# Performance work log

Measured on AMD Instinct MI355X. Metric: run time of the kernel, lower is better.

The kernel has to match this reference:

```python
import jax, jax.numpy as jnp
import numpy as np

HEADS = 8
BN_EPS = 1e-5

def _bn(x2d, g, b):
    # torch BatchNorm1d in training mode: biased batch stats
    mu = x2d.mean(0)
    var = x2d.var(0)
    return (x2d - mu) * jax.lax.rsqrt(var + BN_EPS) * g + b

def _window_indices(H):
    # exclusive-end box coordinates, in the exact order of the torch loop
    m = H // 2
    r0, r1, c0, c1 = [], [], [], []
    for i in range(1, m + 1):
        wins = [(m - i, m + i + 1, m - i, m + i + 1),  # full square
                (m - i, m + 1,     m - i, m + i + 1),  # top half
                (m,     m + i + 1, m - i, m + i + 1),  # bottom half
                (m - i, m + i + 1, m - i, m + 1),      # left half
                (m - i, m + i + 1, m,     m + i + 1)]  # right half
        for a, b, c, d in wins:
            r0.append(a); r1.append(b); c0.append(c); c1.append(d)
    r0 = np.array(r0); r1 = np.array(r1); c0 = np.array(c0); c1 = np.array(c1)
    counts = ((r1 - r0) * (c1 - c0)).astype(np.float32)
    return r0, r1, c0, c1, counts

def _box_sums(P, r0, r1, c0, c1):
    # P: padded 2D prefix sum [B, C, H+1, H+1]; returns [B, C, K]
    return P[:, :, r1, c1] - P[:, :, r0, c1] - P[:, :, r1, c0] + P[:, :, r0, c0]

def _integral(img):
    return jnp.pad(jnp.cumsum(jnp.cumsum(img, axis=2), axis=3), ((0, 0), (0, 0), (1, 0), (1, 0)))

def setup_inputs() -> dict:
    key = jax.random.key(0)
    ks = jax.random.split(key, 8)
    B, Cin, H = 64, 512, 31
    C = 512  # heads * base_dim
    x = jax.random.normal(ks[0], (B, Cin, H, H), dtype=jnp.float32)
    w_v = jax.random.normal(ks[1], (Cin, C), dtype=jnp.float32) * 0.02
    w_k = jax.random.normal(ks[2], (Cin, C), dtype=jnp.float32) * 0.02
    w_fc = jax.random.normal(ks[3], (Cin + C, 512), dtype=jnp.float32) * 0.02
    z = lambda n: jnp.zeros((n,), jnp.float32)
    o = lambda n: jnp.ones((n,), jnp.float32)
    return {"x": x,
            "w_v": w_v, "b_v": z(C), "g_vn": o(C), "b_vn": z(C),
            "w_k": w_k, "b_k": z(C), "g_kn": o(C), "b_kn": z(C),
            "w_fc": w_fc, "b_fc": z(512), "g_fcn": o(512), "b_fcn": z(512)}

def reference(x, w_v, b_v, g_vn, b_vn, w_k, b_k, g_kn, b_kn, w_fc, b_fc, g_fcn, b_fcn):
    B, Cin, H, W = x.shape
    N = H * W
    C = w_v.shape[1]
    d = C // HEADS
    m = H // 2
    xt = x.reshape(B, Cin, N).transpose(0, 2, 1)       # [B, N, Cin]
    x0 = xt[:, N // 2, :]                              # [B, Cin] center pixel feature
    flat = xt.reshape(B * N, Cin)
    v = jax.nn.relu(_bn(flat @ w_v + b_v, g_vn, b_vn))
    v = v.reshape(B, N, C).transpose(0, 2, 1).reshape(B, C, H, H)
    k = _bn(flat @ w_k + b_k, g_kn, b_kn).reshape(B, N, HEADS, d).transpose(0, 2, 1, 3)  # [B,h,N,d]
    q = k[:, :, N // 2, :]                             # [B, h, d]
    attn = jax.nn.softmax(jnp.einsum('bhd,bhnd->bhn', q, k) * (d ** -0.5), axis=-1)      # [B,h,N]
    attn_full = jnp.broadcast_to(attn[:, :, None, :], (B, HEADS, d, N)).reshape(B, C, H, H)
    xw = attn_full * v                                 # attn-weighted values [B,C,H,H]
    eps = 1e-16
    r0, r1, c0, c1, counts = _window_indices(H)
    Px = _integral(xw)
    Pa = _integral(attn_full)
    mx = _box_sums(Px, r0, r1, c0, c1) / counts        # window means of xw   [B,C,K]
    ma = _box_sums(Pa, r0, r1, c0, c1) / counts        # window means of attn [B,C,K]
    y_win = (mx / (ma + eps)).transpose(0, 2, 1)       # [B, K, C]
    y = jnp.concatenate([xw[:, :, m, m][:, None, :], y_win], axis=1)  # [B, n, C]
    # F.normalize(p=2, dim=2)
    y = y / jnp.maximum(jnp.linalg.norm(y, axis=2, keepdims=True), 1e-12)
    n = y.shape[1]
    yy = jnp.concatenate([jnp.broadcast_to(x0[:, None, :], (B, n, Cin)), y], axis=-1)
    out = jax.nn.relu(_bn(yy.reshape(B * n, Cin + C) @ w_fc + b_fc, g_fcn, b_fcn))
    return out.reshape(B, n, -1)
```

## Files before the change

kernel.cpp:

```cpp
#include <hip/hip_runtime.h>
#include <stdint.h>

#define DEV __device__ __forceinline__

typedef __bf16 bf16x8 __attribute__((ext_vector_type(8)));
typedef unsigned short u16x8 __attribute__((ext_vector_type(8)));
typedef float f32x4 __attribute__((ext_vector_type(4)));

DEV uint16_t f2bf(float f) {
    union { float f; uint32_t u; } v; v.f = f;
    uint32_t r = v.u + 0x7fffu + ((v.u >> 16) & 1u);
    return (uint16_t)(r >> 16);
}
DEV float bf2f(uint16_t h) {
    union { uint32_t u; float f; } v; v.u = ((uint32_t)h) << 16;
    return v.f;
}

#if __has_builtin(__builtin_amdgcn_global_load_lds)
DEV void async16(const uint16_t* g, uint16_t* l) {
    __builtin_amdgcn_global_load_lds(
        (const __attribute__((address_space(1))) uint32_t*)g,
        (__attribute__((address_space(3))) uint32_t*)l, 16, 0, 0);
}
#else
DEV void async16(const uint16_t* g, uint16_t* l) {
    *(u16x8*)l = *(const u16x8*)g;
}
#endif

__global__ void k_convert_x(const float* __restrict__ x, uint16_t* __restrict__ xbt) {
    __shared__ float tile[32][33];
    int b = blockIdx.z;
    int n0 = blockIdx.x * 32;
    int c0 = blockIdx.y * 32;
    int tx = threadIdx.x, ty = threadIdx.y;
    #pragma unroll
    for (int i = 0; i < 4; ++i) {
        int c = c0 + ty + 8 * i;
        int n = n0 + tx;
        float v = 0.f;
        if (n < 961) v = x[((size_t)b * 512 + c) * 961 + n];
        tile[ty + 8 * i][tx] = v;
    }
    __syncthreads();
    #pragma unroll
    for (int i = 0; i < 4; ++i) {
        int n = n0 + ty + 8 * i;
        if (n < 961)
            xbt[((size_t)b * 961 + n) * 512 + c0 + tx] = f2bf(tile[tx][ty + 8 * i]);
    }
}

__global__ void k_convert_wvk(const float* __restrict__ wv, const float* __restrict__ wk,
                              uint16_t* __restrict__ wvkt) {
    int idx = blockIdx.x * 256 + threadIdx.x;
    int j = idx >> 9, k = idx & 511;
    float v = (j < 512) ? wv[(size_t)k * 512 + j] : wk[(size_t)k * 512 + (j - 512)];
    wvkt[idx] = f2bf(v);
}
__global__ void k_convert_wfc(const float* __restrict__ wfc, uint16_t* __restrict__ wfct) {
    int idx = blockIdx.x * 256 + threadIdx.x;
    int j = idx >> 10, k = idx & 1023;
    wfct[idx] = f2bf(wfc[(size_t)k * 512 + j]);
}

template<int K, int EPI>
__global__ __launch_bounds__(256, 2)
void k_gemm(const uint16_t* __restrict__ A, const uint16_t* __restrict__ Bt,
            int M_real,
            uint16_t* __restrict__ out_v, uint16_t* __restrict__ out_k,
            float* __restrict__ out_f,
            float* __restrict__ colsum, float* __restrict__ colsq)
{
    __shared__ __align__(16) uint16_t sA[128 * 32];
    __shared__ __align__(16) uint16_t sB[128 * 32];
    __shared__ float sStat[256];

    const int tid = threadIdx.x;
    const int wave = tid >> 6, lane = tid & 63;
    const int quad = lane >> 4, l16 = lane & 15;
    const int m0 = blockIdx.y * 128;
    const int j0 = blockIdx.x * 128;
    const int wm = wave >> 1, wj = wave & 1;

    const f32x4 fzero = {0.f, 0.f, 0.f, 0.f};
    f32x4 acc[4][4];
    #pragma unroll
    for (int i = 0; i < 4; ++i)
        #pragma unroll
        for (int j = 0; j < 4; ++j) acc[i][j] = fzero;

    const int c0 = tid;
    const int mA0 = c0 >> 2, kq0 = c0 & 3;
    const int c1 = tid + 256;
    const int mA1 = c1 >> 2, kq1 = c1 & 3;

    const int KT = K / 32;
    for (int kt = 0; kt < KT; ++kt) {
        const uint16_t* Ak = A + (size_t)m0 * K + kt * 32;
        const uint16_t* Bk = Bt + (size_t)j0 * K + kt * 32;
        async16(Ak + (size_t)mA0 * K + kq0 * 8, &sA[c0 * 8]);
        async16(Bk + (size_t)mA0 * K + kq0 * 8, &sB[c0 * 8]);
        async16(Ak + (size_t)mA1 * K + kq1 * 8, &sA[c1 * 8]);
        async16(Bk + (size_t)mA1 * K + kq1 * 8, &sB[c1 * 8]);
        __syncthreads();
        bf16x8 af[4], bfr[4];
        #pragma unroll
        for (int i = 0; i < 4; ++i) {
            int m = wm * 64 + i * 16 + l16;
            u16x8 r = *(const u16x8*)&sA[m * 32 + quad * 8];
            af[i] = __builtin_bit_cast(bf16x8, r);
        }
        #pragma unroll
        for (int j = 0; j < 4; ++j) {
            int jj = wj * 64 + j * 16 + l16;
            u16x8 r = *(const u16x8*)&sB[jj * 32 + quad * 8];
            bfr[j] = __builtin_bit_cast(bf16x8, r);
        }
        #pragma unroll
        for (int i = 0; i < 4; ++i)
            #pragma unroll
            for (int j = 0; j < 4; ++j)
                acc[i][j] = __builtin_amdgcn_mfma_f32_16x16x32_bf16(af[i], bfr[j], acc[i][j], 0, 0, 0);
        __syncthreads();
    }

    sStat[tid] = 0.f;
    __syncthreads();

    #pragma unroll
    for (int j = 0; j < 4; ++j) {
        const int col_local = wj * 64 + j * 16 + l16;
        const int jg = j0 + col_local;
        float ls = 0.f, lq = 0.f;
        #pragma unroll
        for (int i = 0; i < 4; ++i) {
            const int rbase = m0 + wm * 64 + i * 16 + quad * 4;
            #pragma unroll
            for (int reg = 0; reg < 4; ++reg) {
                const int r = rbase + reg;
                const float val = acc[i][j][reg];
                if (r < M_real) {
                    ls += val; lq += val * val;
                    if constexpr (EPI == 0) {
                        unsigned b = (unsigned)r / 961u;
                        unsigned n = (unsigned)r - b * 961u;
                        uint16_t hv = f2bf(val);
                        if (jg < 512) out_v[((size_t)b * 512 + jg) * 961 + n] = hv;
                        else          out_k[((size_t)b * 512 + (jg - 512)) * 961 + n] = hv;
                    } else {
                        out_f[(size_t)r * 512 + jg] = val;
                    }
                }
            }
        }
        ls += __shfl_xor(ls, 16); lq += __shfl_xor(lq, 16);
        ls += __shfl_xor(ls, 32); lq += __shfl_xor(lq, 32);
        if (quad == 0) {
            atomicAdd(&sStat[col_local], ls);
            atomicAdd(&sStat[128 + col_local], lq);
        }
    }
    __syncthreads();
    if (tid < 128) atomicAdd(&colsum[j0 + tid], sStat[tid]);
    else           atomicAdd(&colsq[j0 + (tid & 127)], sStat[tid]);
}

__global__ void k_bnfin(const float* __restrict__ s, const float* __restrict__ q,
                        const float* __restrict__ g, const float* __restrict__ be,
                        float* __restrict__ a, float* __restrict__ b2, float invM) {
    int j = blockIdx.x * 256 + threadIdx.x;
    float mean = s[j] * invM;
    float var = q[j] * invM - mean * mean;
    float aa = g[j] * rsqrtf(var + 1e-5f);
    a[j] = aa;
    b2[j] = be[j] - mean * aa;
}

__global__ void k_attn(const uint16_t* __restrict__ kraw,
                       const float* __restrict__ avec, const float* __restrict__ bvec,
                       float* __restrict__ attn, float* __restrict__ maw)
{
    __shared__ float qa[64];
    __shared__ float s_qb;
    __shared__ float att[961];
    __shared__ float red[8];

    int bh = blockIdx.x;
    int b = bh >> 3, h = bh & 7;
    int tid = threadIdx.x;

    if (tid < 64) {
        int c = h * 64 + tid;
        float kr = bf2f(kraw[((size_t)b * 512 + c) * 961 + 480]);
        float a = avec[512 + c], bb = bvec[512 + c];
        float qv = kr * a + bb;
        qa[tid] = qv * a;
        float qb = qv * bb;
        for (int off = 32; off; off >>= 1) qb += __shfl_down(qb, off);
        if (tid == 0) s_qb = qb;
    }
    __syncthreads();

    float lg[4];
    float lmax = -1e30f;
    #pragma unroll
    for (int it = 0; it < 4; ++it) {
        int n = tid + it * 256;
        float dot = -1e30f;
        if (n < 961) {
            const uint16_t* kp = kraw + ((size_t)b * 512 + h * 64) * 961 + n;
            float acc = 0.f;
            #pragma unroll 16
            for (int dd = 0; dd < 64; ++dd)
                acc += qa[dd] * bf2f(kp[(size_t)dd * 961]);
            dot = (acc + s_qb) * 0.125f;
        }
        lg[it] = dot;
        lmax = fmaxf(lmax, dot);
    }
    for (int off = 32; off; off >>= 1) lmax = fmaxf(lmax, __shfl_xor(lmax, off));
    if ((tid & 63) == 0) red[tid >> 6] = lmax;
    __syncthreads();
    float bmax = fmaxf(fmaxf(red[0], red[1]), fmaxf(red[2], red[3]));

    float lsum = 0.f;
    #pragma unroll
    for (int it = 0; it < 4; ++it) {
        int n = tid + it * 256;
        if (n < 961) {
            float e = __expf(lg[it] - bmax);
            lg[it] = e;
            lsum += e;
        }
    }
    for (int off = 32; off; off >>= 1) lsum += __shfl_xor(lsum, off);
    if ((tid & 63) == 0) red[4 + (tid >> 6)] = lsum;
    __syncthreads();
    float inv = 1.f / (red[4] + red[5] + red[6] + red[7]);
    #pragma unroll
    for (int it = 0; it < 4; ++it) {
        int n = tid + it * 256;
        if (n < 961) {
            float v = lg[it] * inv;
            att[n] = v;
            attn[(size_t)bh * 961 + n] = v;
        }
    }
    __syncthreads();

    if (tid < 31) { float s = 0.f; for (int cc = 0; cc < 31; ++cc) { s += att[tid * 31 + cc]; att[tid * 31 + cc] = s; } }
    __syncthreads();
    if (tid < 31) { float s = 0.f; for (int rr = 0; rr < 31; ++rr) { s += att[rr * 31 + tid]; att[rr * 31 + tid] = s; } }
    __syncthreads();

    if (tid < 75) {
        int i = tid / 5 + 1, t = tid % 5;
        const int m = 15;
        int r0, r1, cc0, cc1;
        switch (t) {
            case 0: r0 = m - i; r1 = m + i + 1; cc0 = m - i; cc1 = m + i + 1; break;
            case 1: r0 = m - i; r1 = m + 1;     cc0 = m - i; cc1 = m + i + 1; break;
            case 2: r0 = m;     r1 = m + i + 1; cc0 = m - i; cc1 = m + i + 1; break;
            case 3: r0 = m - i; r1 = m + i + 1; cc0 = m - i; cc1 = m + 1;     break;
            default:r0 = m - i; r1 = m + i + 1; cc0 = m;     cc1 = m + i + 1; break;
        }
        auto S = [&](int r, int c) -> float { return (r < 0 || c < 0) ? 0.f : att[r * 31 + c]; };
        float box = S(r1 - 1, cc1 - 1) - S(r0 - 1, cc1 - 1) - S(r1 - 1, cc0 - 1) + S(r0 - 1, cc0 - 1);
        float cnt = (float)((r1 - r0) * (cc1 - cc0));
        maw[(size_t)bh * 75 + tid] = box / cnt;
    }
}

__global__ void k_winbox(const uint16_t* __restrict__ vraw,
                         const float* __restrict__ avec, const float* __restrict__ bvec,
                         const float* __restrict__ attn, const float* __restrict__ maw,
                         float* __restrict__ y)
{
    __shared__ float xw[961];
    __shared__ float s_center;
    int bc = blockIdx.x;
    int b = bc >> 9, c = bc & 511;
    int h = c >> 6;
    int tid = threadIdx.x;
    float a = avec[c], bb = bvec[c];
    const uint16_t* vp = vraw + (size_t)bc * 961;
    const float* ap = attn + (size_t)(b * 8 + h) * 961;
    for (int n = tid; n < 961; n += 128) {
        float v = fmaxf(bf2f(vp[n]) * a + bb, 0.f);
        xw[n] = v * ap[n];
    }
    __syncthreads();
    if (tid == 0) s_center = xw[480];
    __syncthreads();
    if (tid < 31) { float s = 0.f; for (int cc = 0; cc < 31; ++cc) { s += xw[tid * 31 + cc]; xw[tid * 31 + cc] = s; } }
    __syncthreads();
    if (tid < 31) { float s = 0.f; for (int rr = 0; rr < 31; ++rr) { s += xw[rr * 31 + tid]; xw[rr * 31 + tid] = s; } }
    __syncthreads();
    if (tid < 75) {
        int i = tid / 5 + 1, t = tid % 5;
        const int m = 15;
        int r0, r1, cc0, cc1;
        switch (t) {
            case 0: r0 = m - i; r1 = m + i + 1; cc0 = m - i; cc1 = m + i + 1; break;
            case 1: r0 = m - i; r1 = m + 1;     cc0 = m - i; cc1 = m + i + 1; break;
            case 2: r0 = m;     r1 = m + i + 1; cc0 = m - i; cc1 = m + i + 1; break;
            case 3: r0 = m - i; r1 = m + i + 1; cc0 = m - i; cc1 = m + 1;     break;
            default:r0 = m - i; r1 = m + i + 1; cc0 = m;     cc1 = m + i + 1; break;
        }
        auto S = [&](int r, int cc) -> float { return (r < 0 || cc < 0) ? 0.f : xw[r * 31 + cc]; };
        float box = S(r1 - 1, cc1 - 1) - S(r0 - 1, cc1 - 1) - S(r1 - 1, cc0 - 1) + S(r0 - 1, cc0 - 1);
        float cnt = (float)((r1 - r0) * (cc1 - cc0));
        float mx = box / cnt;
        float ma = maw[(size_t)(b * 8 + h) * 75 + tid];
        y[((size_t)b * 76 + 1 + tid) * 512 + c] = mx / (ma + 1e-16f);
    }
    if (tid == 96) y[((size_t)b * 76) * 512 + c] = s_center;
}

__global__ void k_build_yy(const float* __restrict__ y, const float* __restrict__ x,
                           uint16_t* __restrict__ yy)
{
    __shared__ float red[4];
    int row = blockIdx.x;
    int b = row / 76;
    int tid = threadIdx.x;
    const float* yp = y + (size_t)row * 512;
    float v0 = yp[tid], v1 = yp[tid + 256];
    float ss = v0 * v0 + v1 * v1;
    for (int off = 32; off; off >>= 1) ss += __shfl_xor(ss, off);
    if ((tid & 63) == 0) red[tid >> 6] = ss;
    __syncthreads();
    float tot = red[0] + red[1] + red[2] + red[3];
    float inv = 1.f / fmaxf(sqrtf(tot), 1e-12f);
    uint16_t* op = yy + (size_t)row * 1024;
    op[tid]           = f2bf(x[((size_t)b * 512 + tid) * 961 + 480]);
    op[tid + 256]     = f2bf(x[((size_t)b * 512 + tid + 256) * 961 + 480]);
    op[512 + tid]       = f2bf(v0 * inv);
    op[512 + tid + 256] = f2bf(v1 * inv);
}

__global__ void k_fcout(const float* __restrict__ fcraw, const float* __restrict__ a2,
                        const float* __restrict__ b2, float* __restrict__ out)
{
    size_t idx = (size_t)blockIdx.x * 256 + threadIdx.x;
    if (idx < (size_t)4864 * 512) {
        int j = (int)(idx & 511);
        out[idx] = fmaxf(fcraw[idx] * a2[j] + b2[j], 0.f);
    }
}

extern "C" void kernel_launch(void* const* d_in, const int* in_sizes, int n_in,
                              void* d_out, int out_size, void* d_ws, size_t ws_size,
                              hipStream_t stream)
{
    (void)in_sizes; (void)n_in; (void)out_size; (void)ws_size;
    const float* x    = (const float*)d_in[0];
    const float* w_v  = (const float*)d_in[1];
    const float* g_vn = (const float*)d_in[3];
    const float* b_vn = (const float*)d_in[4];
    const float* w_k  = (const float*)d_in[5];
    const float* g_kn = (const float*)d_in[7];
    const float* b_kn = (const float*)d_in[8];
    const float* w_fc = (const float*)d_in[9];
    const float* g_fcn = (const float*)d_in[11];
    const float* b_fcn = (const float*)d_in[12];
    float* out = (float*)d_out;

    char* base = (char*)d_ws;
    size_t off = 0;
    auto alloc = [&](size_t bytes) -> void* {
        void* p = base + off;
        off += (bytes + 255) & ~(size_t)255;
        return p;
    };
    uint16_t* xbt  = (uint16_t*)alloc((size_t)61568 * 512 * 2);
    uint16_t* wvkt = (uint16_t*)alloc((size_t)1024 * 512 * 2);
    uint16_t* wfct = (uint16_t*)alloc((size_t)512 * 1024 * 2);
    uint16_t* vraw = (uint16_t*)alloc((size_t)64 * 512 * 961 * 2);
    uint16_t* kraw = (uint16_t*)alloc((size_t)64 * 512 * 961 * 2);
    float* stats   = (float*)alloc(3072 * 4);
    float* avec    = (float*)alloc(1024 * 4);
    float* bvec    = (float*)alloc(1024 * 4);
    float* a2      = (float*)alloc(512 * 4);
    float* b2fc    = (float*)alloc(512 * 4);
    float* attn    = (float*)alloc((size_t)64 * 8 * 961 * 4);
    float* maw     = (float*)alloc((size_t)64 * 8 * 75 * 4);
    float* y       = (float*)alloc((size_t)64 * 76 * 512 * 4);
    uint16_t* yy   = (uint16_t*)alloc((size_t)4864 * 1024 * 2);
    float* fcraw   = (float*)alloc((size_t)4864 * 512 * 4);

    hipMemsetAsync(stats, 0, 3072 * 4, stream);
    k_convert_x<<<dim3(31, 16, 64), dim3(32, 8), 0, stream>>>(x, xbt);
    k_convert_wvk<<<2048, 256, 0, stream>>>(w_v, w_k, wvkt);
    k_convert_wfc<<<2048, 256, 0, stream>>>(w_fc, wfct);

    k_gemm<512, 0><<<dim3(8, 481), 256, 0, stream>>>(xbt, wvkt, 61504, vraw, kraw, nullptr,
                                                     stats, stats + 1024);
    k_bnfin<<<2, 256, 0, stream>>>(stats,       stats + 1024,       g_vn, b_vn, avec,       bvec,       1.f / 61504.f);
    k_bnfin<<<2, 256, 0, stream>>>(stats + 512, stats + 1024 + 512, g_kn, b_kn, avec + 512, bvec + 512, 1.f / 61504.f);

    k_attn<<<512, 256, 0, stream>>>(kraw, avec, bvec, attn, maw);
    k_winbox<<<64 * 512, 128, 0, stream>>>(vraw, avec, bvec, attn, maw, y);
    k_build_yy<<<4864, 256, 0, stream>>>(y, x, yy);

    k_gemm<1024, 1><<<dim3(4, 38), 256, 0, stream>>>(yy, wfct, 4864, nullptr, nullptr, fcraw,
                                                     stats + 2048, stats + 2560);
    k_bnfin<<<2, 256, 0, stream>>>(stats + 2048, stats + 2560, g_fcn, b_fcn, a2, b2fc, 1.f / 4864.f);
    k_fcout<<<9728, 256, 0, stream>>>(fcraw, a2, b2fc, out);
}
```

Baseline: 514.4 us.

## Stage GEMM epilogue through LDS for coalesced transposed stores and XCD-aware tile order

The first GEMM's epilogue used to write bf16 values straight into the channel-major v/k layout, which gives scattered 2-byte stores. It now packs each 64-column half of the tile into a padded LDS buffer and writes it back so that consecutive threads store consecutive spatial positions, giving coalesced writes. The launch also becomes a 1D grid, remapped so that row-blocks are interleaved across the 8 XCDs and all column blocks of one row-block share an XCD for L2 reuse of A. The cost is extra LDS traffic and barriers, and some blocks launch only to exit early.

```diff
diff --git a/kernel.cpp b/kernel.cpp
--- a/kernel.cpp
+++ b/kernel.cpp
@@ -73,15 +73,25 @@
             float* __restrict__ out_f,
             float* __restrict__ colsum, float* __restrict__ colsq)
 {
-    __shared__ __align__(16) uint16_t sA[128 * 32];
-    __shared__ __align__(16) uint16_t sB[128 * 32];
+    __shared__ __align__(16) uint16_t sbuf[8704];
     __shared__ float sStat[256];
+    uint16_t* sA = sbuf;
+    uint16_t* sB = sbuf + 4096;
 
     const int tid = threadIdx.x;
     const int wave = tid >> 6, lane = tid & 63;
     const int quad = lane >> 4, l16 = lane & 15;
-    const int m0 = blockIdx.y * 128;
-    const int j0 = blockIdx.x * 128;
+    int m0, j0;
+    if constexpr (EPI == 0) {
+        int lin = blockIdx.x;
+        int xcd = lin & 7, rest = lin >> 3;
+        int jb = rest & 7, mhi = rest >> 3;
+        int mb = mhi * 8 + xcd;
+        if (mb >= 481) return;
+        m0 = mb * 128; j0 = jb * 128;
+    } else {
+        m0 = blockIdx.y * 128; j0 = blockIdx.x * 128;
+    }
     const int wm = wave >> 1, wj = wave & 1;
 
     const f32x4 fzero = {0.f, 0.f, 0.f, 0.f};
@@ -143,13 +153,7 @@
                 const float val = acc[i][j][reg];
                 if (r < M_real) {
                     ls += val; lq += val * val;
-                    if constexpr (EPI == 0) {
-                        unsigned b = (unsigned)r / 961u;
-                        unsigned n = (unsigned)r - b * 961u;
-                        uint16_t hv = f2bf(val);
-                        if (jg < 512) out_v[((size_t)b * 512 + jg) * 961 + n] = hv;
-                        else          out_k[((size_t)b * 512 + (jg - 512)) * 961 + n] = hv;
-                    } else {
+                    if constexpr (EPI == 1) {
                         out_f[(size_t)r * 512 + jg] = val;
                     }
                 }
@@ -165,6 +169,44 @@
     __syncthreads();
     if (tid < 128) atomicAdd(&colsum[j0 + tid], sStat[tid]);
     else           atomicAdd(&colsq[j0 + (tid & 127)], sStat[tid]);
+
+    if constexpr (EPI == 0) {
+        const int rr = tid & 127;
+        const int cbase = tid >> 7;
+        const int r = m0 + rr;
+        const bool ok = r < M_real;
+        const unsigned bb_ = (unsigned)r / 961u;
+        const unsigned nn = (unsigned)r - bb_ * 961u;
+        #pragma unroll
+        for (int ch = 0; ch < 2; ++ch) {
+            if (wj == ch) {
+                #pragma unroll
+                for (int j = 0; j < 4; ++j) {
+                    const int c = j * 16 + l16;
+                    #pragma unroll
+                    for (int i = 0; i < 4; ++i) {
+                        const int rloc = wm * 64 + i * 16 + quad * 4;
+                        union { uint16_t h[4]; uint64_t u; } p;
+                        #pragma unroll
+                        for (int reg = 0; reg < 4; ++reg) p.h[reg] = f2bf(acc[i][j][reg]);
+                        *(uint64_t*)&sbuf[c * 136 + rloc] = p.u;
+                    }
+                }
+            }
+            __syncthreads();
+            #pragma unroll
+            for (int it = 0; it < 32; ++it) {
+                const int c = cbase + it * 2;
+                const int jg = j0 + ch * 64 + c;
+                const uint16_t hv = sbuf[c * 136 + rr];
+                if (ok) {
+                    if (jg < 512) out_v[((size_t)bb_ * 512 + jg) * 961 + nn] = hv;
+                    else          out_k[((size_t)bb_ * 512 + (jg - 512)) * 961 + nn] = hv;
+                }
+            }
+            __syncthreads();
+        }
+    }
 }
 
 __global__ void k_bnfin(const float* __restrict__ s, const float* __restrict__ q,
@@ -396,8 +438,8 @@
     k_convert_wvk<<<2048, 256, 0, stream>>>(w_v, w_k, wvkt);
     k_convert_wfc<<<2048, 256, 0, stream>>>(w_fc, wfct);
 
-    k_gemm<512, 0><<<dim3(8, 481), 256, 0, stream>>>(xbt, wvkt, 61504, vraw, kraw, nullptr,
-                                                     stats, stats + 1024);
+    k_gemm<512, 0><<<3904, 256, 0, stream>>>(xbt, wvkt, 61504, vraw, kraw, nullptr,
+                                             stats, stats + 1024);
     k_bnfin<<<2, 256, 0, stream>>>(stats,       stats + 1024,       g_vn, b_vn, avec,       bvec,       1.f / 61504.f);
     k_bnfin<<<2, 256, 0, stream>>>(stats + 512, stats + 1024 + 512, g_kn, b_kn, avec + 512, bvec + 512, 1.f / 61504.f);
 
```

Measured after the change: 487.5 us. -5.2%, faster.
